# Kernel optimization log

Measured on AMD Instinct MI355X. Metric: run time of the kernel, lower is better.

Reference implementation:

```python
import jax, jax.numpy as jnp
import numpy as np

T, B, D, H, F, E = 2048, 2, 1024, 16, 4096, 8
HD = D // H


def layer_norm(x, g, b, eps=1e-5):
    m = x.mean(-1, keepdims=True)
    v = ((x - m) ** 2).mean(-1, keepdims=True)
    return (x - m) * jax.lax.rsqrt(v + eps) * g + b


def setup_inputs() -> dict:
    key = jax.random.key(0)
    ks = jax.random.split(key, 24)
    s = 0.02
    inp = {
        "x": jax.random.normal(ks[0], (T, B, D), jnp.float32),
        # self-attention (fairseq MultiheadAttention)
        "Wq": jax.random.normal(ks[1], (D, D), jnp.float32) * s,
        "bq": jnp.zeros((D,), jnp.float32),
        "Wk": jax.random.normal(ks[2], (D, D), jnp.float32) * s,
        "bk": jnp.zeros((D,), jnp.float32),
        "Wv": jax.random.normal(ks[3], (D, D), jnp.float32) * s,
        "bv": jnp.zeros((D,), jnp.float32),
        "Wo": jax.random.normal(ks[4], (D, D), jnp.float32) * s,
        "bo": jnp.zeros((D,), jnp.float32),
        "ln1_g": jnp.ones((D,), jnp.float32),
        "ln1_b": jnp.zeros((D,), jnp.float32),
        "ln2_g": jnp.ones((D,), jnp.float32),
        "ln2_b": jnp.zeros((D,), jnp.float32),
        # MoE: expert_centroids Linear(D -> E, bias=False) => weight [E, D]
        "cent": jax.random.normal(ks[5], (E, D), jnp.float32) * s,
        # per-expert MoESublayer params (base_sublayers=1)
        "e_ln_g": jnp.ones((E, D), jnp.float32),
        "e_ln_b": jnp.zeros((E, D), jnp.float32),
        "e_W1": jax.random.normal(ks[6], (E, D, F), jnp.float32) * s,
        "e_b1": jnp.zeros((E, F), jnp.float32),
        "e_W2": jax.random.normal(ks[7], (E, F, D), jnp.float32) * s,
        "e_b2": jnp.zeros((E, D), jnp.float32),
    }
    return inp


def reference(x, Wq, bq, Wk, bk, Wv, bv, Wo, bo, ln1_g, ln1_b, ln2_g, ln2_b,
              cent, e_ln_g, e_ln_b, e_W1, e_b1, e_W2, e_b2):
    # ---- self-attention block (pre-norm, causal) ----
    res = x  # [T,B,D]
    h = layer_norm(x, ln1_g, ln1_b)
    q = ((h @ Wq) + bq) * (HD ** -0.5)
    k = h @ Wk + bk
    v = h @ Wv + bv
    q = q.reshape(T, B, H, HD)
    k = k.reshape(T, B, H, HD)
    v = v.reshape(T, B, H, HD)
    scores = jnp.einsum('tbhd,sbhd->bhts', q, k)
    causal = jnp.tril(jnp.ones((T, T), bool))
    scores = jnp.where(causal, scores, -1e9)
    p = jax.nn.softmax(scores, axis=-1)
    a = jnp.einsum('bhts,sbhd->tbhd', p, v).reshape(T, B, D)
    x = res + (a @ Wo + bo)

    # ---- MoE block (pre-norm) ----
    res = x
    h = layer_norm(x, ln2_g, ln2_b)
    # MoELayer: transpose(0,1) then flatten -> [B*T, D] token-major by batch
    xs = h.transpose(1, 0, 2).reshape(B * T, D)
    logits = xs.astype(jnp.float32) @ cent.T  # fp32 gating, [N,E]
    assign = jnp.argmax(logits, axis=-1)      # greedy top-1 routing

    # single-device semantics: All2All identity; sort + inverse-sort cancel,
    # so out[t] = expert_{assign[t]}(xs[t]). Compute each expert densely and select.
    def sublayer(g, b, W1, b1, W2, b2):
        hh = jax.nn.relu(layer_norm(xs, g, b) @ W1 + b1)  # [N,F]
        return xs + hh @ W2 + b2                          # internal residual

    ys = jax.vmap(sublayer)(e_ln_g, e_ln_b, e_W1, e_b1, e_W2, e_b2)  # [E,N,D]
    moe_out = jnp.take_along_axis(ys, assign[None, :, None], axis=0)[0]  # [N,D]
    moe_out = moe_out.reshape(B, T, D).transpose(1, 0, 2)  # back to [T,B,D]

    return res + moe_out
```

## Files before the change

### kernel.cpp

```cpp
#include <hip/hip_runtime.h>
#include <hip/hip_bf16.h>
#include <math.h>

#define T_ 2048
#define B_ 2
#define D_ 1024
#define H_ 16
#define F_ 4096
#define E_ 8
#define N_ 4096
#define HD_ 64
#define PADROWS 5120

typedef __attribute__((ext_vector_type(8))) short short8_t;
typedef __attribute__((ext_vector_type(4))) float f32x4_t;

__device__ __forceinline__ unsigned short f2bf(float f) {
    union { float f; unsigned u; } a; a.f = f;
    unsigned r = a.u + 0x7FFFu + ((a.u >> 16) & 1u);
    return (unsigned short)(r >> 16);
}

__device__ __forceinline__ void glds16(const unsigned short* g, unsigned short* l) {
    __builtin_amdgcn_global_load_lds(
        (const __attribute__((address_space(1))) void*)g,
        (__attribute__((address_space(3))) void*)l, 16, 0, 0);
}

__device__ __forceinline__ void blockReduce2(float& a, float& b, float* sm) {
    #pragma unroll
    for (int m = 32; m; m >>= 1) { a += __shfl_xor(a, m); b += __shfl_xor(b, m); }
    const int w = threadIdx.x >> 6, l = threadIdx.x & 63;
    __syncthreads();
    if (l == 0) { sm[w] = a; sm[8 + w] = b; }
    __syncthreads();
    a = sm[0] + sm[1] + sm[2] + sm[3];
    b = sm[8] + sm[9] + sm[10] + sm[11];
}

__global__ __launch_bounds__(256) void k_transpose(const float* __restrict__ in,
                                                   unsigned short* __restrict__ out,
                                                   int R, int C) {
    __shared__ float tile[32][33];
    const int c0 = blockIdx.x * 32, r0 = blockIdx.y * 32;
    const size_t base = (size_t)blockIdx.z * R * C;
    in += base; out += base;
    const int tx = threadIdx.x & 31, ty = threadIdx.x >> 5;
    #pragma unroll
    for (int i = 0; i < 32; i += 8)
        tile[ty + i][tx] = in[(size_t)(r0 + ty + i) * C + c0 + tx];
    __syncthreads();
    #pragma unroll
    for (int i = 0; i < 32; i += 8)
        out[(size_t)(c0 + ty + i) * R + r0 + tx] = f2bf(tile[tx][ty + i]);
}

__global__ __launch_bounds__(256) void k_transpose_v(const unsigned short* __restrict__ in,
                                                     unsigned short* __restrict__ out) {
    const int bh = blockIdx.x;
    const int t0 = blockIdx.y * 128;
    const int tid = threadIdx.x;
    const int hd = tid & 63;
    const size_t ib = (size_t)bh * T_ * HD_;
    const size_t ob = (size_t)bh * HD_ * T_;
    for (int tb = tid >> 6; tb < 16; tb += 4) {
        const int t = t0 + tb * 8;
        short8_t v;
        #pragma unroll
        for (int k = 0; k < 8; ++k)
            v[k] = (short)in[ib + (size_t)(t + k) * HD_ + hd];
        *(short8_t*)(out + ob + (size_t)hd * T_ + t) = v;
    }
}

__global__ __launch_bounds__(256) void k_ln(const float* __restrict__ x,
                                            const float* __restrict__ g,
                                            const float* __restrict__ b,
                                            unsigned short* __restrict__ out) {
    __shared__ float sm[16];
    const int row = blockIdx.x, tid = threadIdx.x;
    const float4 v = *(const float4*)(x + (size_t)row * D_ + tid * 4);
    float s1 = v.x + v.y + v.z + v.w;
    float s2 = v.x * v.x + v.y * v.y + v.z * v.z + v.w * v.w;
    blockReduce2(s1, s2, sm);
    const float mean = s1 * (1.f / D_);
    const float inv  = rsqrtf(s2 * (1.f / D_) - mean * mean + 1e-5f);
    const float4 gg = *(const float4*)(g + tid * 4);
    const float4 bb = *(const float4*)(b + tid * 4);
    unsigned long long pk =
          (unsigned long long)f2bf((v.x - mean) * inv * gg.x + bb.x)
        | ((unsigned long long)f2bf((v.y - mean) * inv * gg.y + bb.y) << 16)
        | ((unsigned long long)f2bf((v.z - mean) * inv * gg.z + bb.z) << 32)
        | ((unsigned long long)f2bf((v.w - mean) * inv * gg.w + bb.w) << 48);
    *(unsigned long long*)(out + (size_t)row * D_ + tid * 4) = pk;
}

__device__ __forceinline__ void gemm_core(const unsigned short* ap0, const unsigned short* ap1,
                                          const unsigned short* bp0, const unsigned short* bp1,
                                          int K, unsigned short* Als, unsigned short* Bls,
                                          f32x4_t (&acc)[4][4]) {
    const int tid = threadIdx.x, w = tid >> 6, l = tid & 63;
    const int wm = (w >> 1) * 64, wn = (w & 1) * 64;
    const int fr = l & 15, fg = (l >> 4) * 8;
    f32x4_t z4 = {0.f, 0.f, 0.f, 0.f};
    #pragma unroll
    for (int m = 0; m < 4; m++)
        #pragma unroll
        for (int n = 0; n < 4; n++) acc[m][n] = z4;
    for (int k0 = 0; k0 < K; k0 += 32) {
        __syncthreads();
        glds16(ap0, Als + w * 512);
        glds16(ap1, Als + (w + 4) * 512);
        glds16(bp0, Bls + w * 512);
        glds16(bp1, Bls + (w + 4) * 512);
        ap0 += 32; ap1 += 32; bp0 += 32; bp1 += 32;
        __syncthreads();
        short8_t a[4], b[4];
        #pragma unroll
        for (int m = 0; m < 4; m++) a[m] = *(const short8_t*)(Als + (wm + m * 16 + fr) * 32 + fg);
        #pragma unroll
        for (int n = 0; n < 4; n++) b[n] = *(const short8_t*)(Bls + (wn + n * 16 + fr) * 32 + fg);
        #pragma unroll
        for (int m = 0; m < 4; m++)
            #pragma unroll
            for (int n = 0; n < 4; n++)
                acc[m][n] = __builtin_amdgcn_mfma_f32_16x16x32_bf16(a[m], b[n], acc[m][n], 0, 0, 0);
    }
}

__global__ __launch_bounds__(256) void k_gemm_qkv(
    const unsigned short* __restrict__ A, const unsigned short* __restrict__ BT,
    const float* __restrict__ bq, const float* __restrict__ bk, const float* __restrict__ bv,
    unsigned short* __restrict__ Qb, unsigned short* __restrict__ Kb, unsigned short* __restrict__ Vb) {
    __shared__ unsigned short Als[4096], Bls[4096];
    const int tid = threadIdx.x, w = tid >> 6, l = tid & 63;
    const int row0 = blockIdx.x * 128, col0 = blockIdx.y * 128;
    const int r0s = w * 16 + (l >> 2), r1s = 64 + w * 16 + (l >> 2), cs = (l & 3) * 8;
    const unsigned short* ap0 = A + (size_t)(row0 + r0s) * D_ + cs;
    const unsigned short* ap1 = A + (size_t)(row0 + r1s) * D_ + cs;
    const unsigned short* bp0 = BT + (size_t)(col0 + r0s) * D_ + cs;
    const unsigned short* bp1 = BT + (size_t)(col0 + r1s) * D_ + cs;
    f32x4_t acc[4][4];
    gemm_core(ap0, ap1, bp0, bp1, D_, Als, Bls, acc);
    const int wm = (w >> 1) * 64, wn = (w & 1) * 64, fr = l & 15, fg4 = l >> 4;
    #pragma unroll
    for (int n = 0; n < 4; n++) {
        const int gcol = col0 + wn + n * 16 + fr;
        const int which = gcol >> 10, dc = gcol & 1023;
        const float bias = which == 0 ? bq[dc] : (which == 1 ? bk[dc] : bv[dc]);
        unsigned short* dst = which == 0 ? Qb : (which == 1 ? Kb : Vb);
        const int hh = dc >> 6, hd = dc & 63;
        #pragma unroll
        for (int m = 0; m < 4; m++)
            #pragma unroll
            for (int rr = 0; rr < 4; rr++) {
                const int grow = row0 + wm + m * 16 + fg4 * 4 + rr;
                float v = acc[m][n][rr] + bias;
                if (which == 0) v *= 0.1803368801111204f;
                const int t = grow >> 1, bb = grow & 1;
                dst[((size_t)(bb * H_ + hh) * T_ + t) * HD_ + hd] = f2bf(v);
            }
    }
}

__global__ __launch_bounds__(256) void k_attn(const unsigned short* __restrict__ Qb,
                                              const unsigned short* __restrict__ Kb,
                                              const unsigned short* __restrict__ Vt,
                                              unsigned short* __restrict__ aout) {
    __shared__ unsigned short Kl[2][4096];
    __shared__ unsigned short Vl[2][4096];
    __shared__ unsigned short Pl[4][32][72];
    const int id = blockIdx.x;
    const int qt = (id < 256) ? (15 - (id & 15)) : (id & 15);
    const int bh = (id >> 4) & 31;
    const int tid = threadIdx.x, w = tid >> 6, l = tid & 63;
    const int fr = l & 15, fg4 = l >> 4;
    const int row0 = w * 8 + (l >> 3);
    const int swz = ((l & 7) ^ (l >> 3)) * 8;
    const size_t base = (size_t)bh * T_ * HD_;
    const unsigned short* Qp = Qb + base;
    const unsigned short* kps = Kb + base + (size_t)row0 * HD_ + swz;
    const unsigned short* vps = Vt + base + (size_t)row0 * T_ + swz;
    const int qw0 = qt * 128 + w * 32;

    short8_t aq[2][2];
    #pragma unroll
    for (int m = 0; m < 2; ++m)
        #pragma unroll
        for (int kk = 0; kk < 2; ++kk)
            aq[m][kk] = *(const short8_t*)(Qp + (size_t)(qw0 + m * 16 + fr) * HD_ + kk * 32 + fg4 * 8);

    f32x4_t z4 = {0.f, 0.f, 0.f, 0.f};
    f32x4_t accO[2][4];
    float mrun[2][4], lrun[2][4];
    #pragma unroll
    for (int m = 0; m < 2; ++m)
        #pragma unroll
        for (int i = 0; i < 4; ++i) { accO[m][i] = z4; mrun[m][i] = -1e30f; lrun[m][i] = 0.f; }

    const int niter = (qt + 1) * 2;

    glds16(kps,            &Kl[0][w * 512]);
    glds16(kps + 32 * HD_, &Kl[0][2048 + w * 512]);
    glds16(vps,            &Vl[0][w * 512]);
    glds16(vps + 32 * T_,  &Vl[0][2048 + w * 512]);
    asm volatile("s_waitcnt vmcnt(0)" ::: "memory");
    __syncthreads();

    for (int it = 0; it < niter; ++it) {
        const int cur = it & 1;
        const int s0 = it * 64;
        if (it + 1 < niter) {
            const size_t ko = (size_t)(it + 1) * 64 * HD_;
            const int vo = (it + 1) * 64;
            glds16(kps + ko,            &Kl[cur ^ 1][w * 512]);
            glds16(kps + ko + 32 * HD_, &Kl[cur ^ 1][2048 + w * 512]);
            glds16(vps + vo,            &Vl[cur ^ 1][w * 512]);
            glds16(vps + vo + 32 * T_,  &Vl[cur ^ 1][2048 + w * 512]);
        }
        if (s0 <= qw0 + 31) {
            const unsigned short* KT = &Kl[cur][0];
            const unsigned short* VT = &Vl[cur][0];

            f32x4_t sc[2][4];
            #pragma unroll
            for (int m = 0; m < 2; ++m)
                #pragma unroll
                for (int n = 0; n < 4; ++n) sc[m][n] = z4;
            #pragma unroll
            for (int n = 0; n < 4; ++n)
                #pragma unroll
                for (int kk = 0; kk < 2; ++kk) {
                    const int row = n * 16 + fr;
                    const short8_t bk = *(const short8_t*)(KT + row * 64 + ((kk * 32 + fg4 * 8) ^ ((fr & 7) << 3)));
                    sc[0][n] = __builtin_amdgcn_mfma_f32_16x16x32_bf16(aq[0][kk], bk, sc[0][n], 0, 0, 0);
                    sc[1][n] = __builtin_amdgcn_mfma_f32_16x16x32_bf16(aq[1][kk], bk, sc[1][n], 0, 0, 0);
                }

            const bool domask = (s0 + 63 > qw0);
            #pragma unroll
            for (int m = 0; m < 2; ++m)
                #pragma unroll
                for (int rr = 0; rr < 4; ++rr) {
                    const int q = qw0 + m * 16 + fg4 * 4 + rr;
                    float v[4];
                    #pragma unroll
                    for (int n = 0; n < 4; ++n) v[n] = sc[m][n][rr];
                    if (domask) {
                        #pragma unroll
                        for (int n = 0; n < 4; ++n)
                            if (s0 + n * 16 + fr > q) v[n] = -1e30f;
                    }
                    float mx = fmaxf(fmaxf(v[0], v[1]), fmaxf(v[2], v[3]));
                    mx = fmaxf(mx, __shfl_xor(mx, 1));
                    mx = fmaxf(mx, __shfl_xor(mx, 2));
                    mx = fmaxf(mx, __shfl_xor(mx, 4));
                    mx = fmaxf(mx, __shfl_xor(mx, 8));
                    const float mnew = fmaxf(mrun[m][rr], mx);
                    const float scl = exp2f(mrun[m][rr] - mnew);
                    float p[4], rs = 0.f;
                    #pragma unroll
                    for (int n = 0; n < 4; ++n) { p[n] = exp2f(v[n] - mnew); rs += p[n]; }
                    rs += __shfl_xor(rs, 1); rs += __shfl_xor(rs, 2);
                    rs += __shfl_xor(rs, 4); rs += __shfl_xor(rs, 8);
                    lrun[m][rr] = lrun[m][rr] * scl + rs;
                    mrun[m][rr] = mnew;
                    #pragma unroll
                    for (int hf = 0; hf < 4; ++hf) accO[m][hf][rr] *= scl;
                    #pragma unroll
                    for (int n = 0; n < 4; ++n)
                        Pl[w][m * 16 + fg4 * 4 + rr][n * 16 + fr] = f2bf(p[n]);
                }

            asm volatile("s_waitcnt lgkmcnt(0)" ::: "memory");
            __builtin_amdgcn_sched_barrier(0);

            #pragma unroll
            for (int kks = 0; kks < 2; ++kks) {
                const short8_t pa0 = *(const short8_t*)(&Pl[w][fr][kks * 32 + fg4 * 8]);
                const short8_t pa1 = *(const short8_t*)(&Pl[w][16 + fr][kks * 32 + fg4 * 8]);
                #pragma unroll
                for (int hf = 0; hf < 4; ++hf) {
                    const int row = hf * 16 + fr;
                    const short8_t bv = *(const short8_t*)(VT + row * 64 + ((kks * 32 + fg4 * 8) ^ ((fr & 7) << 3)));
                    accO[0][hf] = __builtin_amdgcn_mfma_f32_16x16x32_bf16(pa0, bv, accO[0][hf], 0, 0, 0);
                    accO[1][hf] = __builtin_amdgcn_mfma_f32_16x16x32_bf16(pa1, bv, accO[1][hf], 0, 0, 0);
                }
            }
        }
        asm volatile("s_waitcnt vmcnt(0)" ::: "memory");
        __syncthreads();
    }

    const int bidx = bh >> 4, hidx = bh & 15;
    #pragma unroll
    for (int m = 0; m < 2; ++m) {
        float linv[4];
        #pragma unroll
        for (int rr = 0; rr < 4; ++rr) linv[rr] = 1.f / lrun[m][rr];
        #pragma unroll
        for (int hf = 0; hf < 4; ++hf)
            #pragma unroll
            for (int rr = 0; rr < 4; ++rr) {
                const int q = qw0 + m * 16 + fg4 * 4 + rr;
                const float o = accO[m][hf][rr] * linv[rr];
                const int row = q * B_ + bidx;
                const int col = hidx * 64 + hf * 16 + fr;
                aout[(size_t)row * D_ + col] = f2bf(o);
            }
    }
}

__global__ __launch_bounds__(256) void k_gemm_o(
    const unsigned short* __restrict__ A, const unsigned short* __restrict__ BT,
    const float* __restrict__ bo, const float* __restrict__ xin, float* __restrict__ x2) {
    __shared__ unsigned short Als[4096], Bls[4096];
    const int tid = threadIdx.x, w = tid >> 6, l = tid & 63;
    const int row0 = blockIdx.x * 128, col0 = blockIdx.y * 128;
    const int r0s = w * 16 + (l >> 2), r1s = 64 + w * 16 + (l >> 2), cs = (l & 3) * 8;
    const unsigned short* ap0 = A + (size_t)(row0 + r0s) * D_ + cs;
    const unsigned short* ap1 = A + (size_t)(row0 + r1s) * D_ + cs;
    const unsigned short* bp0 = BT + (size_t)(col0 + r0s) * D_ + cs;
    const unsigned short* bp1 = BT + (size_t)(col0 + r1s) * D_ + cs;
    f32x4_t acc[4][4];
    gemm_core(ap0, ap1, bp0, bp1, D_, Als, Bls, acc);
    const int wm = (w >> 1) * 64, wn = (w & 1) * 64, fr = l & 15, fg4 = l >> 4;
    #pragma unroll
    for (int n = 0; n < 4; n++) {
        const int gcol = col0 + wn + n * 16 + fr;
        const float bias = bo[gcol];
        #pragma unroll
        for (int m = 0; m < 4; m++)
            #pragma unroll
            for (int rr = 0; rr < 4; rr++) {
                const int grow = row0 + wm + m * 16 + fg4 * 4 + rr;
                const size_t idx = (size_t)grow * D_ + gcol;
                x2[idx] = xin[idx] + acc[m][n][rr] + bias;
            }
    }
}

__global__ __launch_bounds__(256) void k_ln2_gate(
    float* __restrict__ x2, const float* __restrict__ g2, const float* __restrict__ b2,
    const float* __restrict__ cent, const float* __restrict__ eg, const float* __restrict__ eb,
    unsigned short* __restrict__ z, int* __restrict__ assign, int* __restrict__ counts) {
    __shared__ float sm[48];
    const int row = blockIdx.x, tid = threadIdx.x;
    const int w = tid >> 6, l = tid & 63;
    float* xr = x2 + (size_t)row * D_;
    const float4 v = *(const float4*)(xr + tid * 4);
    float s1 = v.x + v.y + v.z + v.w;
    float s2 = v.x * v.x + v.y * v.y + v.z * v.z + v.w * v.w;
    blockReduce2(s1, s2, sm);
    const float mean = s1 * (1.f / D_);
    const float inv  = rsqrtf(s2 * (1.f / D_) - mean * mean + 1e-5f);
    const float4 gg = *(const float4*)(g2 + tid * 4), bb = *(const float4*)(b2 + tid * 4);
    float4 u;
    u.x = (v.x - mean) * inv * gg.x + bb.x;
    u.y = (v.y - mean) * inv * gg.y + bb.y;
    u.z = (v.z - mean) * inv * gg.z + bb.z;
    u.w = (v.w - mean) * inv * gg.w + bb.w;
    float p[E_];
    #pragma unroll
    for (int e = 0; e < E_; e++) {
        const float4 c = *(const float4*)(cent + (size_t)e * D_ + tid * 4);
        p[e] = u.x * c.x + u.y * c.y + u.z * c.z + u.w * c.w;
    }
    #pragma unroll
    for (int m = 32; m; m >>= 1)
        #pragma unroll
        for (int e = 0; e < E_; e++) p[e] += __shfl_xor(p[e], m);
    __syncthreads();
    if (l == 0) {
        #pragma unroll
        for (int e = 0; e < E_; e++) sm[16 + e * 4 + w] = p[e];
    }
    __syncthreads();
    int best = 0; float bl = -1e30f;
    #pragma unroll
    for (int e = 0; e < E_; e++) {
        const float le = sm[16 + e * 4] + sm[16 + e * 4 + 1] + sm[16 + e * 4 + 2] + sm[16 + e * 4 + 3];
        if (le > bl) { bl = le; best = e; }
    }
    float t1 = u.x + u.y + u.z + u.w;
    float t2 = u.x * u.x + u.y * u.y + u.z * u.z + u.w * u.w;
    blockReduce2(t1, t2, sm);
    const float m2   = t1 * (1.f / D_);
    const float inv2 = rsqrtf(t2 * (1.f / D_) - m2 * m2 + 1e-5f);
    const float4 egv = *(const float4*)(eg + (size_t)best * D_ + tid * 4);
    const float4 ebv = *(const float4*)(eb + (size_t)best * D_ + tid * 4);
    unsigned long long pk =
          (unsigned long long)f2bf((u.x - m2) * inv2 * egv.x + ebv.x)
        | ((unsigned long long)f2bf((u.y - m2) * inv2 * egv.y + ebv.y) << 16)
        | ((unsigned long long)f2bf((u.z - m2) * inv2 * egv.z + ebv.z) << 32)
        | ((unsigned long long)f2bf((u.w - m2) * inv2 * egv.w + ebv.w) << 48);
    *(unsigned long long*)(z + (size_t)row * D_ + tid * 4) = pk;
    float4 xu; xu.x = v.x + u.x; xu.y = v.y + u.y; xu.z = v.z + u.z; xu.w = v.w + u.w;
    *(float4*)(xr + tid * 4) = xu;
    if (tid == 0) { assign[row] = best; atomicAdd(&counts[best], 1); }
}

__global__ void k_init(int* counts, int* cursor, int* perm) {
    const int t = threadIdx.x;
    if (t < E_) { counts[t] = 0; cursor[t] = 0; }
    for (int i = t; i < PADROWS; i += 256) perm[i] = -1;
}

__global__ void k_offsets(const int* counts, int* pad_off) {
    if (threadIdx.x == 0) {
        int o = 0; pad_off[0] = 0;
        for (int e = 0; e < E_; e++) { o += ((counts[e] + 127) >> 7) << 7; pad_off[e + 1] = o; }
    }
}

__global__ void k_scatter(const int* assign, const int* pad_off, int* cursor, int* perm) {
    const int r = blockIdx.x * 256 + threadIdx.x;
    if (r >= N_) return;
    const int e = assign[r];
    const int pos = pad_off[e] + atomicAdd(&cursor[e], 1);
    perm[pos] = r;
}

__global__ __launch_bounds__(256) void k_gemm_e1(
    const unsigned short* __restrict__ z, const unsigned short* __restrict__ W1T,
    const float* __restrict__ eb1, const int* __restrict__ pad_off,
    const int* __restrict__ perm, unsigned short* __restrict__ Y1) {
    __shared__ unsigned short Als[4096], Bls[4096];
    const int tid = threadIdx.x, w = tid >> 6, l = tid & 63;
    const int row0 = blockIdx.x * 128, col0 = blockIdx.y * 128;
    if (row0 >= pad_off[E_]) return;
    int e = 0;
    while (row0 >= pad_off[e + 1]) e++;
    const int r0s = w * 16 + (l >> 2), r1s = 64 + w * 16 + (l >> 2), cs = (l & 3) * 8;
    int pr0 = perm[row0 + r0s]; if (pr0 < 0) pr0 = 0;
    int pr1 = perm[row0 + r1s]; if (pr1 < 0) pr1 = 0;
    const unsigned short* ap0 = z + (size_t)pr0 * D_ + cs;
    const unsigned short* ap1 = z + (size_t)pr1 * D_ + cs;
    const unsigned short* BTe = W1T + (size_t)e * F_ * D_;
    const unsigned short* bp0 = BTe + (size_t)(col0 + r0s) * D_ + cs;
    const unsigned short* bp1 = BTe + (size_t)(col0 + r1s) * D_ + cs;
    f32x4_t acc[4][4];
    gemm_core(ap0, ap1, bp0, bp1, D_, Als, Bls, acc);
    const float* b1e = eb1 + (size_t)e * F_;
    const int wm = (w >> 1) * 64, wn = (w & 1) * 64, fr = l & 15, fg4 = l >> 4;
    #pragma unroll
    for (int n = 0; n < 4; n++) {
        const int gcol = col0 + wn + n * 16 + fr;
        const float bias = b1e[gcol];
        #pragma unroll
        for (int m = 0; m < 4; m++)
            #pragma unroll
            for (int rr = 0; rr < 4; rr++) {
                const int grow = row0 + wm + m * 16 + fg4 * 4 + rr;
                Y1[(size_t)grow * F_ + gcol] = f2bf(fmaxf(acc[m][n][rr] + bias, 0.f));
            }
    }
}

__global__ __launch_bounds__(256) void k_gemm_e2(
    const unsigned short* __restrict__ Y1, const unsigned short* __restrict__ W2T,
    const float* __restrict__ eb2, const int* __restrict__ pad_off,
    const int* __restrict__ perm, const float* __restrict__ x2u, float* __restrict__ out) {
    __shared__ unsigned short Als[4096], Bls[4096];
    const int tid = threadIdx.x, w = tid >> 6, l = tid & 63;
    const int row0 = blockIdx.x * 128, col0 = blockIdx.y * 128;
    if (row0 >= pad_off[E_]) return;
    int e = 0;
    while (row0 >= pad_off[e + 1]) e++;
    const int r0s = w * 16 + (l >> 2), r1s = 64 + w * 16 + (l >> 2), cs = (l & 3) * 8;
    const unsigned short* ap0 = Y1 + (size_t)(row0 + r0s) * F_ + cs;
    const unsigned short* ap1 = Y1 + (size_t)(row0 + r1s) * F_ + cs;
    const unsigned short* BTe = W2T + (size_t)e * D_ * F_;
    const unsigned short* bp0 = BTe + (size_t)(col0 + r0s) * F_ + cs;
    const unsigned short* bp1 = BTe + (size_t)(col0 + r1s) * F_ + cs;
    f32x4_t acc[4][4];
    gemm_core(ap0, ap1, bp0, bp1, F_, Als, Bls, acc);
    const float* b2e = eb2 + (size_t)e * D_;
    const int wm = (w >> 1) * 64, wn = (w & 1) * 64, fr = l & 15, fg4 = l >> 4;
    #pragma unroll
    for (int n = 0; n < 4; n++) {
        const int gcol = col0 + wn + n * 16 + fr;
        const float bias = b2e[gcol];
        #pragma unroll
        for (int m = 0; m < 4; m++)
            #pragma unroll
            for (int rr = 0; rr < 4; rr++) {
                const int grow = row0 + wm + m * 16 + fg4 * 4 + rr;
                const int rdst = perm[grow];
                if (rdst >= 0) {
                    const size_t idx = (size_t)rdst * D_ + gcol;
                    out[idx] = x2u[idx] + acc[m][n][rr] + bias;
                }
            }
    }
}

extern "C" void kernel_launch(void* const* d_in, const int* in_sizes, int n_in,
                              void* d_out, int out_size, void* d_ws, size_t ws_size,
                              hipStream_t stream) {
    const float* x    = (const float*)d_in[0];
    const float* Wq   = (const float*)d_in[1];
    const float* bq   = (const float*)d_in[2];
    const float* Wk   = (const float*)d_in[3];
    const float* bk   = (const float*)d_in[4];
    const float* Wv   = (const float*)d_in[5];
    const float* bv   = (const float*)d_in[6];
    const float* Wo   = (const float*)d_in[7];
    const float* bo   = (const float*)d_in[8];
    const float* ln1g = (const float*)d_in[9];
    const float* ln1b = (const float*)d_in[10];
    const float* ln2g = (const float*)d_in[11];
    const float* ln2b = (const float*)d_in[12];
    const float* cent = (const float*)d_in[13];
    const float* egw  = (const float*)d_in[14];
    const float* ebw  = (const float*)d_in[15];
    const float* eW1  = (const float*)d_in[16];
    const float* eb1  = (const float*)d_in[17];
    const float* eW2  = (const float*)d_in[18];
    const float* eb2  = (const float*)d_in[19];
    float* out = (float*)d_out;

    char* W = (char*)d_ws;
    unsigned short* WqkvT = (unsigned short*)(W);
    unsigned short* WoT   = (unsigned short*)(W + 6291456);
    unsigned short* Qb    = (unsigned short*)(W + 8388608);
    unsigned short* Kb    = (unsigned short*)(W + 16777216);
    unsigned short* Vb    = (unsigned short*)(W + 25165824);
    unsigned short* aout  = (unsigned short*)(W + 33554432);
    unsigned short* Y1    = (unsigned short*)(W);
    unsigned short* W1T   = (unsigned short*)(W + 41943040);
    unsigned short* W2T   = (unsigned short*)(W + 109051904);
    unsigned short* h1z   = (unsigned short*)(W + 176160768);
    float*          x2    = (float*)(W + 184549376);
    unsigned short* Vt    = (unsigned short*)(W + 201326592);
    int*            assign= (int*)(W + 209715200);
    int*            perm  = (int*)(W + 209731584);
    int*            counts= (int*)(W + 209752064);
    int*            cursor= (int*)(W + 209752192);
    int*            pad_off=(int*)(W + 209752320);

    k_transpose<<<dim3(32, 32, 1), 256, 0, stream>>>(Wq, WqkvT,               1024, 1024);
    k_transpose<<<dim3(32, 32, 1), 256, 0, stream>>>(Wk, WqkvT + 1024 * 1024, 1024, 1024);
    k_transpose<<<dim3(32, 32, 1), 256, 0, stream>>>(Wv, WqkvT + 2048 * 1024, 1024, 1024);
    k_transpose<<<dim3(32, 32, 1), 256, 0, stream>>>(Wo, WoT,                 1024, 1024);
    k_transpose<<<dim3(128, 32, 8), 256, 0, stream>>>(eW1, W1T, 1024, 4096);
    k_transpose<<<dim3(32, 128, 8), 256, 0, stream>>>(eW2, W2T, 4096, 1024);

    k_init<<<1, 256, 0, stream>>>(counts, cursor, perm);
    k_ln<<<N_, 256, 0, stream>>>(x, ln1g, ln1b, h1z);
    k_gemm_qkv<<<dim3(32, 24), 256, 0, stream>>>(h1z, WqkvT, bq, bk, bv, Qb, Kb, Vb);
    k_transpose_v<<<dim3(32, 16), 256, 0, stream>>>(Vb, Vt);
    k_attn<<<dim3(512), 256, 0, stream>>>(Qb, Kb, Vt, aout);
    k_gemm_o<<<dim3(32, 8), 256, 0, stream>>>(aout, WoT, bo, x, x2);
    k_ln2_gate<<<N_, 256, 0, stream>>>(x2, ln2g, ln2b, cent, egw, ebw, h1z, assign, counts);
    k_offsets<<<1, 64, 0, stream>>>(counts, pad_off);
    k_scatter<<<16, 256, 0, stream>>>(assign, pad_off, cursor, perm);
    k_gemm_e1<<<dim3(40, 32), 256, 0, stream>>>(h1z, W1T, eb1, pad_off, perm, Y1);
    k_gemm_e2<<<dim3(40, 8), 256, 0, stream>>>(Y1, W2T, eb2, pad_off, perm, x2, out);
}
```

Before: 578.8 us.

## Rewrite attention with transposed 32x32 MFMA keeping P in registers

The flash-attention kernel now computes S^T = K·Q^T with 32x32x16 bf16 MFMAs, so each lane owns a single query row. The row max and sum then need only one cross-lane shuffle instead of four-step reductions. P is packed with v_cvt_pk_bf16_f32 and exchanged between half-waves by shuffles to form the PV operand, which removes the LDS round trip for P and its waitcnt barrier. Output stores become 64-bit packed writes. The risks are higher register pressure from the 16-wide accumulators and score arrays, and correctness depending on the MFMA lane layout being right.

```diff
diff --git a/kernel.cpp b/kernel.cpp
--- a/kernel.cpp
+++ b/kernel.cpp
@@ -14,11 +14,19 @@
 
 typedef __attribute__((ext_vector_type(8))) short short8_t;
 typedef __attribute__((ext_vector_type(4))) float f32x4_t;
+typedef __attribute__((ext_vector_type(16))) float f32x16_t;
+typedef __attribute__((ext_vector_type(4))) unsigned u32x4_t;
 
 __device__ __forceinline__ unsigned short f2bf(float f) {
     union { float f; unsigned u; } a; a.f = f;
     unsigned r = a.u + 0x7FFFu + ((a.u >> 16) & 1u);
     return (unsigned short)(r >> 16);
+}
+
+__device__ __forceinline__ unsigned cvtpk(float lo, float hi) {
+    unsigned r;
+    asm("v_cvt_pk_bf16_f32 %0, %1, %2" : "=v"(r) : "v"(lo), "v"(hi));
+    return r;
 }
 
 __device__ __forceinline__ void glds16(const unsigned short* g, unsigned short* l) {
@@ -169,12 +177,11 @@
                                               unsigned short* __restrict__ aout) {
     __shared__ unsigned short Kl[2][4096];
     __shared__ unsigned short Vl[2][4096];
-    __shared__ unsigned short Pl[4][32][72];
     const int id = blockIdx.x;
     const int qt = (id < 256) ? (15 - (id & 15)) : (id & 15);
     const int bh = (id >> 4) & 31;
     const int tid = threadIdx.x, w = tid >> 6, l = tid & 63;
-    const int fr = l & 15, fg4 = l >> 4;
+    const int q5 = l & 31, hi = l >> 5, l7 = l & 7;
     const int row0 = w * 8 + (l >> 3);
     const int swz = ((l & 7) ^ (l >> 3)) * 8;
     const size_t base = (size_t)bh * T_ * HD_;
@@ -182,21 +189,17 @@
     const unsigned short* kps = Kb + base + (size_t)row0 * HD_ + swz;
     const unsigned short* vps = Vt + base + (size_t)row0 * T_ + swz;
     const int qw0 = qt * 128 + w * 32;
-
-    short8_t aq[2][2];
-    #pragma unroll
-    for (int m = 0; m < 2; ++m)
-        #pragma unroll
-        for (int kk = 0; kk < 2; ++kk)
-            aq[m][kk] = *(const short8_t*)(Qp + (size_t)(qw0 + m * 16 + fr) * HD_ + kk * 32 + fg4 * 8);
-
-    f32x4_t z4 = {0.f, 0.f, 0.f, 0.f};
-    f32x4_t accO[2][4];
-    float mrun[2][4], lrun[2][4];
-    #pragma unroll
-    for (int m = 0; m < 2; ++m)
-        #pragma unroll
-        for (int i = 0; i < 4; ++i) { accO[m][i] = z4; mrun[m][i] = -1e30f; lrun[m][i] = 0.f; }
+    const int q = qw0 + q5;
+
+    short8_t aq[4];
+    #pragma unroll
+    for (int khd = 0; khd < 4; ++khd)
+        aq[khd] = *(const short8_t*)(Qp + (size_t)q * HD_ + khd * 16 + hi * 8);
+
+    f32x16_t accO0, accO1;
+    #pragma unroll
+    for (int i = 0; i < 16; ++i) { accO0[i] = 0.f; accO1[i] = 0.f; }
+    float mrun = -1e30f, lrun = 0.f;
 
     const int niter = (qt + 1) * 2;
 
@@ -219,95 +222,104 @@
             glds16(vps + vo + 32 * T_,  &Vl[cur ^ 1][2048 + w * 512]);
         }
         if (s0 <= qw0 + 31) {
-            const unsigned short* KT = &Kl[cur][0];
-            const unsigned short* VT = &Vl[cur][0];
-
-            f32x4_t sc[2][4];
-            #pragma unroll
-            for (int m = 0; m < 2; ++m)
-                #pragma unroll
-                for (int n = 0; n < 4; ++n) sc[m][n] = z4;
-            #pragma unroll
-            for (int n = 0; n < 4; ++n)
-                #pragma unroll
-                for (int kk = 0; kk < 2; ++kk) {
-                    const int row = n * 16 + fr;
-                    const short8_t bk = *(const short8_t*)(KT + row * 64 + ((kk * 32 + fg4 * 8) ^ ((fr & 7) << 3)));
-                    sc[0][n] = __builtin_amdgcn_mfma_f32_16x16x32_bf16(aq[0][kk], bk, sc[0][n], 0, 0, 0);
-                    sc[1][n] = __builtin_amdgcn_mfma_f32_16x16x32_bf16(aq[1][kk], bk, sc[1][n], 0, 0, 0);
+            const unsigned short* KT = Kl[cur];
+            const unsigned short* VT = Vl[cur];
+
+            f32x16_t st0, st1;
+            #pragma unroll
+            for (int i = 0; i < 16; ++i) { st0[i] = 0.f; st1[i] = 0.f; }
+            #pragma unroll
+            for (int khd = 0; khd < 4; ++khd) {
+                const int cb = (khd * 16 + hi * 8) ^ (l7 * 8);
+                const short8_t k0 = *(const short8_t*)(KT + q5 * 64 + cb);
+                const short8_t k1 = *(const short8_t*)(KT + (32 + q5) * 64 + cb);
+                st0 = __builtin_amdgcn_mfma_f32_32x32x16_bf16(k0, aq[khd], st0, 0, 0, 0);
+                st1 = __builtin_amdgcn_mfma_f32_32x32x16_bf16(k1, aq[khd], st1, 0, 0, 0);
+            }
+
+            const bool domask = (s0 + 63 > qw0);
+            float pmax = -3e38f;
+            #pragma unroll
+            for (int r = 0; r < 16; ++r) {
+                float v0 = st0[r], v1 = st1[r];
+                if (domask) {
+                    const int kv0 = s0 + (r & 3) + 8 * (r >> 2) + 4 * hi;
+                    if (kv0 > q)      v0 = -1e30f;
+                    if (kv0 + 32 > q) v1 = -1e30f;
                 }
-
-            const bool domask = (s0 + 63 > qw0);
-            #pragma unroll
-            for (int m = 0; m < 2; ++m)
-                #pragma unroll
-                for (int rr = 0; rr < 4; ++rr) {
-                    const int q = qw0 + m * 16 + fg4 * 4 + rr;
-                    float v[4];
-                    #pragma unroll
-                    for (int n = 0; n < 4; ++n) v[n] = sc[m][n][rr];
-                    if (domask) {
-                        #pragma unroll
-                        for (int n = 0; n < 4; ++n)
-                            if (s0 + n * 16 + fr > q) v[n] = -1e30f;
-                    }
-                    float mx = fmaxf(fmaxf(v[0], v[1]), fmaxf(v[2], v[3]));
-                    mx = fmaxf(mx, __shfl_xor(mx, 1));
-                    mx = fmaxf(mx, __shfl_xor(mx, 2));
-                    mx = fmaxf(mx, __shfl_xor(mx, 4));
-                    mx = fmaxf(mx, __shfl_xor(mx, 8));
-                    const float mnew = fmaxf(mrun[m][rr], mx);
-                    const float scl = exp2f(mrun[m][rr] - mnew);
-                    float p[4], rs = 0.f;
-                    #pragma unroll
-                    for (int n = 0; n < 4; ++n) { p[n] = exp2f(v[n] - mnew); rs += p[n]; }
-                    rs += __shfl_xor(rs, 1); rs += __shfl_xor(rs, 2);
-                    rs += __shfl_xor(rs, 4); rs += __shfl_xor(rs, 8);
-                    lrun[m][rr] = lrun[m][rr] * scl + rs;
-                    mrun[m][rr] = mnew;
-                    #pragma unroll
-                    for (int hf = 0; hf < 4; ++hf) accO[m][hf][rr] *= scl;
-                    #pragma unroll
-                    for (int n = 0; n < 4; ++n)
-                        Pl[w][m * 16 + fg4 * 4 + rr][n * 16 + fr] = f2bf(p[n]);
-                }
-
-            asm volatile("s_waitcnt lgkmcnt(0)" ::: "memory");
-            __builtin_amdgcn_sched_barrier(0);
-
-            #pragma unroll
-            for (int kks = 0; kks < 2; ++kks) {
-                const short8_t pa0 = *(const short8_t*)(&Pl[w][fr][kks * 32 + fg4 * 8]);
-                const short8_t pa1 = *(const short8_t*)(&Pl[w][16 + fr][kks * 32 + fg4 * 8]);
-                #pragma unroll
-                for (int hf = 0; hf < 4; ++hf) {
-                    const int row = hf * 16 + fr;
-                    const short8_t bv = *(const short8_t*)(VT + row * 64 + ((kks * 32 + fg4 * 8) ^ ((fr & 7) << 3)));
-                    accO[0][hf] = __builtin_amdgcn_mfma_f32_16x16x32_bf16(pa0, bv, accO[0][hf], 0, 0, 0);
-                    accO[1][hf] = __builtin_amdgcn_mfma_f32_16x16x32_bf16(pa1, bv, accO[1][hf], 0, 0, 0);
-                }
+                st0[r] = v0; st1[r] = v1;
+                pmax = fmaxf(pmax, fmaxf(v0, v1));
+            }
+            pmax = fmaxf(pmax, __shfl_xor(pmax, 32));
+            const float mnew = fmaxf(mrun, pmax);
+            const float scl = exp2f(mrun - mnew);
+            float pt0[16], pt1[16];
+            float rs = 0.f;
+            #pragma unroll
+            for (int r = 0; r < 16; ++r) {
+                pt0[r] = exp2f(st0[r] - mnew);
+                pt1[r] = exp2f(st1[r] - mnew);
+                rs += pt0[r] + pt1[r];
+            }
+            rs += __shfl_xor(rs, 32);
+            lrun = lrun * scl + rs;
+            mrun = mnew;
+            #pragma unroll
+            for (int i = 0; i < 16; ++i) { accO0[i] *= scl; accO1[i] *= scl; }
+
+            unsigned Wp[2][4][2];
+            #pragma unroll
+            for (int b = 0; b < 4; ++b) {
+                Wp[0][b][0] = cvtpk(pt0[4 * b + 0], pt0[4 * b + 1]);
+                Wp[0][b][1] = cvtpk(pt0[4 * b + 2], pt0[4 * b + 3]);
+                Wp[1][b][0] = cvtpk(pt1[4 * b + 0], pt1[4 * b + 1]);
+                Wp[1][b][1] = cvtpk(pt1[4 * b + 2], pt1[4 * b + 3]);
+            }
+
+            #pragma unroll
+            for (int ks = 0; ks < 4; ++ks) {
+                const int t = ks >> 1, b0 = (ks & 1) * 2;
+                const unsigned ownA0 = Wp[t][b0][0],     ownA1 = Wp[t][b0][1];
+                const unsigned ownB0 = Wp[t][b0 + 1][0], ownB1 = Wp[t][b0 + 1][1];
+                const unsigned send0 = hi ? ownA0 : ownB0;
+                const unsigned send1 = hi ? ownA1 : ownB1;
+                const unsigned recv0 = __shfl_xor(send0, 32);
+                const unsigned recv1 = __shfl_xor(send1, 32);
+                u32x4_t wds;
+                wds[0] = hi ? recv0 : ownA0;
+                wds[1] = hi ? recv1 : ownA1;
+                wds[2] = hi ? ownB0 : recv0;
+                wds[3] = hi ? ownB1 : recv1;
+                const short8_t pfrag = __builtin_bit_cast(short8_t, wds);
+                const int cb = (ks * 16 + hi * 8) ^ (l7 * 8);
+                const short8_t v0 = *(const short8_t*)(VT + q5 * 64 + cb);
+                const short8_t v1 = *(const short8_t*)(VT + (32 + q5) * 64 + cb);
+                accO0 = __builtin_amdgcn_mfma_f32_32x32x16_bf16(v0, pfrag, accO0, 0, 0, 0);
+                accO1 = __builtin_amdgcn_mfma_f32_32x32x16_bf16(v1, pfrag, accO1, 0, 0, 0);
             }
         }
         asm volatile("s_waitcnt vmcnt(0)" ::: "memory");
         __syncthreads();
     }
 
+    const float linv = 1.f / lrun;
     const int bidx = bh >> 4, hidx = bh & 15;
-    #pragma unroll
-    for (int m = 0; m < 2; ++m) {
-        float linv[4];
-        #pragma unroll
-        for (int rr = 0; rr < 4; ++rr) linv[rr] = 1.f / lrun[m][rr];
-        #pragma unroll
-        for (int hf = 0; hf < 4; ++hf)
-            #pragma unroll
-            for (int rr = 0; rr < 4; ++rr) {
-                const int q = qw0 + m * 16 + fg4 * 4 + rr;
-                const float o = accO[m][hf][rr] * linv[rr];
-                const int row = q * B_ + bidx;
-                const int col = hidx * 64 + hf * 16 + fr;
-                aout[(size_t)row * D_ + col] = f2bf(o);
-            }
+    unsigned short* orow = aout + (size_t)(q * B_ + bidx) * D_ + hidx * 64;
+    #pragma unroll
+    for (int g = 0; g < 4; ++g) {
+        const int hd0 = 8 * g + 4 * hi;
+        unsigned long long pk0 =
+              (unsigned long long)f2bf(accO0[4 * g + 0] * linv)
+            | ((unsigned long long)f2bf(accO0[4 * g + 1] * linv) << 16)
+            | ((unsigned long long)f2bf(accO0[4 * g + 2] * linv) << 32)
+            | ((unsigned long long)f2bf(accO0[4 * g + 3] * linv) << 48);
+        *(unsigned long long*)(orow + hd0) = pk0;
+        unsigned long long pk1 =
+              (unsigned long long)f2bf(accO1[4 * g + 0] * linv)
+            | ((unsigned long long)f2bf(accO1[4 * g + 1] * linv) << 16)
+            | ((unsigned long long)f2bf(accO1[4 * g + 2] * linv) << 32)
+            | ((unsigned long long)f2bf(accO1[4 * g + 3] * linv) << 48);
+        *(unsigned long long*)(orow + 32 + hd0) = pk1;
     }
 }
 
```

After: 525.2 us. 9.3% less time.
